# Performance work log

Hardware: AMD Instinct MI355X
Metric: run time of the kernel (lower is better)

## Reference

```python
import jax, jax.numpy as jnp
import numpy as np

B, A, G = 16, 262144, 128


def _make_boxes(key, shape):
    # boxes in (x1, y1, x2, y2) with strictly positive width/height
    k1, k2 = jax.random.split(key)
    cxy = jax.random.uniform(k1, shape[:-1] + (2,), minval=0.0, maxval=1024.0)
    wh = jax.random.uniform(k2, shape[:-1] + (2,), minval=8.0, maxval=256.0)
    return jnp.concatenate([cxy - 0.5 * wh, cxy + 0.5 * wh], axis=-1).astype(jnp.float32)


def setup_inputs() -> dict:
    key = jax.random.key(0)
    k1, k2, k3, k4 = jax.random.split(key, 4)
    bbox_regression = jax.random.normal(k1, (B, A, 4), dtype=jnp.float32)
    anchors = _make_boxes(k2, (A, 4))
    gt_boxes = _make_boxes(k3, (B, G, 4))
    # values in [-2, G): negatives are background/ignored, >=0 index into gt_boxes
    matched_idxs = jax.random.randint(k4, (B, A), -2, G, dtype=jnp.int32)
    return {
        "bbox_regression": bbox_regression,
        "anchors": anchors,
        "gt_boxes": gt_boxes,
        "matched_idxs": matched_idxs,
    }


def _encode(gt, anchors):
    # torchvision BoxCoder.encode_single with weights (1, 1, 1, 1)
    ex_w = anchors[..., 2] - anchors[..., 0]
    ex_h = anchors[..., 3] - anchors[..., 1]
    ex_cx = anchors[..., 0] + 0.5 * ex_w
    ex_cy = anchors[..., 1] + 0.5 * ex_h
    gt_w = gt[..., 2] - gt[..., 0]
    gt_h = gt[..., 3] - gt[..., 1]
    gt_cx = gt[..., 0] + 0.5 * gt_w
    gt_cy = gt[..., 1] + 0.5 * gt_h
    dx = (gt_cx - ex_cx) / ex_w
    dy = (gt_cy - ex_cy) / ex_h
    dw = jnp.log(gt_w / ex_w)
    dh = jnp.log(gt_h / ex_h)
    return jnp.stack([dx, dy, dw, dh], axis=-1)


def reference(bbox_regression, anchors, gt_boxes, matched_idxs):
    fg = matched_idxs >= 0                                  # [B, A] foreground mask
    idx = jnp.maximum(matched_idxs, 0)                      # clamp for safe gather
    matched_gt = jnp.take_along_axis(gt_boxes, idx[..., None], axis=1)  # [B, A, 4]
    target_regression = _encode(matched_gt, anchors[None, :, :])        # [B, A, 4]
    l1 = jnp.sum(jnp.abs(bbox_regression - target_regression), axis=-1)  # [B, A]
    l1 = jnp.where(fg, l1, 0.0)
    num_fg = jnp.sum(fg, axis=1)                            # [B]
    per_image = jnp.sum(l1, axis=1) / jnp.maximum(1, num_fg).astype(l1.dtype)
    return jnp.sum(per_image) / max(1, B)
```

## Files before the change

kernel.cpp:

```cpp
#include <hip/hip_runtime.h>
#include <math.h>

#define BB 16
#define AA 262144
#define GG 128
#define TPB 256
#define NBLK (AA / TPB)
#define RT  1024


__global__ __launch_bounds__(TPB, 3) void loss_main_kernel(
    const float4* __restrict__ reg,
    const float4* __restrict__ anc,
    const float4* __restrict__ gt,
    const int*   __restrict__ mi,
    float2* __restrict__ ws)
{
    __shared__ float4 gts[BB * GG];
    __shared__ float  S[BB][TPB];
    __shared__ float  redC[BB * 4];

    const int t  = threadIdx.x;
    const int bx = blockIdx.x;
    const int a  = bx * TPB + t;

    float4 gload[(BB * GG) / TPB];
#pragma unroll
    for (int i = 0; i < (BB * GG) / TPB; ++i)
        gload[i] = gt[i * TPB + t];

    int mjv[BB];
#pragma unroll
    for (int b = 0; b < BB; ++b) mjv[b] = mi[b * AA + a];

    float4 r[BB];
#pragma unroll
    for (int b = 0; b < BB; ++b) r[b] = reg[b * AA + a];

    const float4 an = anc[a];

#pragma unroll
    for (int i = 0; i < (BB * GG) / TPB; ++i) {
        const float4 g = gload[i];
        const float w = g.z - g.x;
        const float h = g.w - g.y;
        gts[i * TPB + t] = make_float4(g.x + 0.5f * w, g.y + 0.5f * h,
                                       __logf(w), __logf(h));
    }

    const float ex_w  = an.z - an.x;
    const float ex_h  = an.w - an.y;
    const float ex_cx = an.x + 0.5f * ex_w;
    const float ex_cy = an.y + 0.5f * ex_h;
    const float inv_w = 1.0f / ex_w;
    const float inv_h = 1.0f / ex_h;
    const float lw    = __logf(ex_w);
    const float lh    = __logf(ex_h);

    __syncthreads();

    const int wv   = t >> 6;
    const int lane = t & 63;

#pragma unroll
    for (int b = 0; b < BB; ++b) {
        const int mj = mjv[b];
        const float4 g = gts[b * GG + (mj < 0 ? 0 : mj)];

        const float dx = (g.x - ex_cx) * inv_w;
        const float dy = (g.y - ex_cy) * inv_h;
        const float dw = g.z - lw;
        const float dh = g.w - lh;

        const float l1 = fabsf(r[b].x - dx) + fabsf(r[b].y - dy) +
                         fabsf(r[b].z - dw) + fabsf(r[b].w - dh);

        S[b][t] = (mj >= 0) ? l1 : 0.0f;

        const unsigned long long bal = __ballot(mj >= 0);
        if (lane == 0) redC[b * 4 + wv] = (float)__popcll(bal);
    }
    __syncthreads();

    {
        const int b = t >> 4;
        const int c = t & 15;
        float p = 0.0f;
#pragma unroll
        for (int j = 0; j < 16; ++j) p += S[b][c + 16 * j];
#pragma unroll
        for (int o = 8; o > 0; o >>= 1) p += __shfl_down(p, o);
        if (c == 0) {
            const float cnt = redC[b * 4] + redC[b * 4 + 1] +
                              redC[b * 4 + 2] + redC[b * 4 + 3];
            ws[b * NBLK + bx] = make_float2(p, cnt);
        }
    }
}

__global__ __launch_bounds__(RT) void reduce_final_kernel(
    const float2* __restrict__ ws,
    float* __restrict__ out)
{
    __shared__ float per_img[BB];
    const int t    = threadIdx.x;
    const int wv   = t >> 6;
    const int lane = t & 63;

    const float4* w4 = (const float4*)ws;
    float s = 0.0f, c = 0.0f;
#pragma unroll
    for (int k = 0; k < 8; ++k) {
        const float4 v = w4[wv * 512 + k * 64 + lane];
        s += v.x + v.z;
        c += v.y + v.w;
    }
#pragma unroll
    for (int o = 32; o > 0; o >>= 1) {
        s += __shfl_down(s, o);
        c += __shfl_down(c, o);
    }
    if (lane == 0) per_img[wv] = s / fmaxf(1.0f, c);
    __syncthreads();

    if (t == 0) {
        float acc = 0.0f;
#pragma unroll
        for (int b = 0; b < BB; ++b) acc += per_img[b];
        out[0] = acc / (float)BB;
    }
}

extern "C" void kernel_launch(void* const* d_in, const int* in_sizes, int n_in,
                              void* d_out, int out_size, void* d_ws, size_t ws_size,
                              hipStream_t stream) {
    const float4* reg = (const float4*)d_in[0];
    const float4* anc = (const float4*)d_in[1];
    const float4* gt  = (const float4*)d_in[2];
    const int*    mi  = (const int*)d_in[3];

    float2* ws = (float2*)d_ws;

    loss_main_kernel<<<NBLK, TPB, 0, stream>>>(reg, anc, gt, mi, ws);
    reduce_final_kernel<<<1, RT, 0, stream>>>(ws, (float*)d_out);
}
```

Measured before the change: 111.1 us.

## Fuse final reduction into main kernel via cooperative grid sync, two anchors per thread

Replaces the two-kernel launch with a single cooperative kernel in which each thread handles two anchors, halving the block count to 512, and block 0 performs the final reduction after a grid-wide sync. This removes the second kernel launch and amortizes the per-block ground-truth smem preload over more anchors. The cost is doubled register pressure (occupancy hint lowered to 2), the grid-sync overhead, and the requirement that all 512 blocks be co-resident. If the cooperative launch fails, the original two-kernel path runs instead.

Result: slower. 216.0 us (+94.4%).

```diff
diff --git a/kernel.cpp b/kernel.cpp
--- a/kernel.cpp
+++ b/kernel.cpp
@@ -1,13 +1,156 @@
 #include <hip/hip_runtime.h>
+#include <hip/hip_cooperative_groups.h>
 #include <math.h>
+
+namespace cg = cooperative_groups;
 
 #define BB 16
 #define AA 262144
 #define GG 128
 #define TPB 256
-#define NBLK (AA / TPB)
-#define RT  1024
-
+
+#define APBF 512
+#define NBF  (AA / APBF)
+
+#define NBK  (AA / TPB)
+#define RT   1024
+
+__global__ __launch_bounds__(TPB, 2) void loss_fused(
+    const float4* __restrict__ reg,
+    const float4* __restrict__ anc,
+    const float4* __restrict__ gt,
+    const int*   __restrict__ mi,
+    float2* __restrict__ ws,
+    float* __restrict__ out)
+{
+    __shared__ float4 gts[BB * GG];
+    __shared__ float  S[BB][TPB];
+    __shared__ float  redC[BB * 4];
+    __shared__ float  per_img[BB];
+
+    const int t  = threadIdx.x;
+    const int bx = blockIdx.x;
+    const int a0 = bx * APBF + t;
+    const int a1 = a0 + TPB;
+
+    float4 gload[(BB * GG) / TPB];
+#pragma unroll
+    for (int i = 0; i < (BB * GG) / TPB; ++i)
+        gload[i] = gt[i * TPB + t];
+
+    int mj0[BB], mj1[BB];
+#pragma unroll
+    for (int b = 0; b < BB; ++b) mj0[b] = mi[b * AA + a0];
+#pragma unroll
+    for (int b = 0; b < BB; ++b) mj1[b] = mi[b * AA + a1];
+
+    float4 r0[BB], r1[BB];
+#pragma unroll
+    for (int b = 0; b < BB; ++b) r0[b] = reg[b * AA + a0];
+#pragma unroll
+    for (int b = 0; b < BB; ++b) r1[b] = reg[b * AA + a1];
+
+    const float4 an0 = anc[a0];
+    const float4 an1 = anc[a1];
+
+#pragma unroll
+    for (int i = 0; i < (BB * GG) / TPB; ++i) {
+        const float4 g = gload[i];
+        const float w = g.z - g.x;
+        const float h = g.w - g.y;
+        gts[i * TPB + t] = make_float4(g.x + 0.5f * w, g.y + 0.5f * h,
+                                       __logf(w), __logf(h));
+    }
+
+    const float ew0 = an0.z - an0.x, eh0 = an0.w - an0.y;
+    const float cx0 = an0.x + 0.5f * ew0, cy0 = an0.y + 0.5f * eh0;
+    const float iw0 = 1.0f / ew0, ih0 = 1.0f / eh0;
+    const float lw0 = __logf(ew0), lh0 = __logf(eh0);
+
+    const float ew1 = an1.z - an1.x, eh1 = an1.w - an1.y;
+    const float cx1 = an1.x + 0.5f * ew1, cy1 = an1.y + 0.5f * eh1;
+    const float iw1 = 1.0f / ew1, ih1 = 1.0f / eh1;
+    const float lw1 = __logf(ew1), lh1 = __logf(eh1);
+
+    __syncthreads();
+
+    const int wv   = t >> 6;
+    const int lane = t & 63;
+
+#pragma unroll
+    for (int b = 0; b < BB; ++b) {
+        const int m0 = mj0[b];
+        const int m1 = mj1[b];
+        const float4 g0 = gts[b * GG + (m0 < 0 ? 0 : m0)];
+        const float4 g1 = gts[b * GG + (m1 < 0 ? 0 : m1)];
+
+        const float l1a = fabsf(r0[b].x - (g0.x - cx0) * iw0) +
+                          fabsf(r0[b].y - (g0.y - cy0) * ih0) +
+                          fabsf(r0[b].z - (g0.z - lw0)) +
+                          fabsf(r0[b].w - (g0.w - lh0));
+        const float l1b = fabsf(r1[b].x - (g1.x - cx1) * iw1) +
+                          fabsf(r1[b].y - (g1.y - cy1) * ih1) +
+                          fabsf(r1[b].z - (g1.z - lw1)) +
+                          fabsf(r1[b].w - (g1.w - lh1));
+
+        S[b][t] = ((m0 >= 0) ? l1a : 0.0f) + ((m1 >= 0) ? l1b : 0.0f);
+
+        const unsigned long long bal0 = __ballot(m0 >= 0);
+        const unsigned long long bal1 = __ballot(m1 >= 0);
+        if (lane == 0)
+            redC[b * 4 + wv] = (float)(__popcll(bal0) + __popcll(bal1));
+    }
+    __syncthreads();
+
+    {
+        const int b = t >> 4;
+        const int c = t & 15;
+        float p = 0.0f;
+#pragma unroll
+        for (int j = 0; j < 16; ++j) p += S[b][c + 16 * j];
+#pragma unroll
+        for (int o = 8; o > 0; o >>= 1) p += __shfl_down(p, o);
+        if (c == 0) {
+            const float cnt = redC[b * 4] + redC[b * 4 + 1] +
+                              redC[b * 4 + 2] + redC[b * 4 + 3];
+            ws[b * NBF + bx] = make_float2(p, cnt);
+        }
+    }
+
+    __threadfence();
+    cg::this_grid().sync();
+    if (bx != 0) return;
+    __threadfence();
+
+    {
+        const float4* w4 = (const float4*)ws;
+#pragma unroll
+        for (int k = 0; k < 4; ++k) {
+            const int b = wv * 4 + k;
+            float s = 0.0f, c = 0.0f;
+#pragma unroll
+            for (int j = 0; j < 4; ++j) {
+                const float4 v = w4[b * 256 + j * 64 + lane];
+                s += v.x + v.z;
+                c += v.y + v.w;
+            }
+#pragma unroll
+            for (int o = 32; o > 0; o >>= 1) {
+                s += __shfl_down(s, o);
+                c += __shfl_down(c, o);
+            }
+            if (lane == 0) per_img[b] = s / fmaxf(1.0f, c);
+        }
+    }
+    __syncthreads();
+
+    if (t == 0) {
+        float acc = 0.0f;
+#pragma unroll
+        for (int b = 0; b < BB; ++b) acc += per_img[b];
+        out[0] = acc / (float)BB;
+    }
+}
 
 __global__ __launch_bounds__(TPB, 3) void loss_main_kernel(
     const float4* __restrict__ reg,
@@ -93,7 +236,7 @@
         if (c == 0) {
             const float cnt = redC[b * 4] + redC[b * 4 + 1] +
                               redC[b * 4 + 2] + redC[b * 4 + 3];
-            ws[b * NBLK + bx] = make_float2(p, cnt);
+            ws[b * NBK + bx] = make_float2(p, cnt);
         }
     }
 }
@@ -138,9 +281,18 @@
     const float4* anc = (const float4*)d_in[1];
     const float4* gt  = (const float4*)d_in[2];
     const int*    mi  = (const int*)d_in[3];
-
-    float2* ws = (float2*)d_ws;
-
-    loss_main_kernel<<<NBLK, TPB, 0, stream>>>(reg, anc, gt, mi, ws);
-    reduce_final_kernel<<<1, RT, 0, stream>>>(ws, (float*)d_out);
-}
+    float2*       ws  = (float2*)d_ws;
+    float*        o   = (float*)d_out;
+
+    void* args[] = {(void*)&reg, (void*)&anc, (void*)&gt,
+                    (void*)&mi, (void*)&ws, (void*)&o};
+    const hipError_t e = hipLaunchCooperativeKernel(
+        reinterpret_cast<void*>(loss_fused), dim3(NBF), dim3(TPB),
+        args, 0, stream);
+
+    if (e != hipSuccess) {
+        (void)hipGetLastError();
+        loss_main_kernel<<<NBK, TPB, 0, stream>>>(reg, anc, gt, mi, ws);
+        reduce_final_kernel<<<1, RT, 0, stream>>>(ws, o);
+    }
+}
```

## Fuse final reduction into main kernel via block-0 spin-wait on per-block tags

Applied to the files above, without the earlier changes.

Drops the separate reduction kernel launch. Each block publishes its partials and then release-stores a tag derived from the previous output value. Block 0 spins until all 1024 tags match, then reduces the partials and writes the result. This removes a kernel launch and its gap, but block 0 busy-waits while holding a CU slot. Correctness depends on the tag changing between calls (it is derived from the old out value) and on all blocks being co-resident or scheduled eventually; the 1<<20 iteration cap limits how long it can hang.

Result: slower. 188.3 us (+69.5%).

```diff
diff --git a/kernel.cpp b/kernel.cpp
--- a/kernel.cpp
+++ b/kernel.cpp
@@ -6,23 +6,30 @@
 #define GG 128
 #define TPB 256
 #define NBLK (AA / TPB)
-#define RT  1024
+
+typedef unsigned long long ull;
 
 
-__global__ __launch_bounds__(TPB, 3) void loss_main_kernel(
+__global__ __launch_bounds__(TPB, 3) void loss_fused_spin(
     const float4* __restrict__ reg,
     const float4* __restrict__ anc,
     const float4* __restrict__ gt,
     const int*   __restrict__ mi,
-    float2* __restrict__ ws)
+    float2* __restrict__ ws_part,
+    ull*    __restrict__ ws_tag,
+    float* __restrict__ out)
 {
     __shared__ float4 gts[BB * GG];
     __shared__ float  S[BB][TPB];
     __shared__ float  redC[BB * 4];
+    __shared__ float  per_img[BB];
 
     const int t  = threadIdx.x;
     const int bx = blockIdx.x;
     const int a  = bx * TPB + t;
+
+    const unsigned eb = __float_as_uint(out[0]);
+    const ull tagv = ((ull)(eb ^ 0x9E3779B9u) << 32) | (ull)(eb ^ 0x7F4A7C15u);
 
     float4 gload[(BB * GG) / TPB];
 #pragma unroll
@@ -93,34 +100,56 @@
         if (c == 0) {
             const float cnt = redC[b * 4] + redC[b * 4 + 1] +
                               redC[b * 4 + 2] + redC[b * 4 + 3];
-            ws[b * NBLK + bx] = make_float2(p, cnt);
+            ws_part[b * NBLK + bx] = make_float2(p, cnt);
         }
     }
-}
 
-__global__ __launch_bounds__(RT) void reduce_final_kernel(
-    const float2* __restrict__ ws,
-    float* __restrict__ out)
-{
-    __shared__ float per_img[BB];
-    const int t    = threadIdx.x;
-    const int wv   = t >> 6;
-    const int lane = t & 63;
+    __syncthreads();
+    if (t == 0) {
+        __threadfence();
+        __hip_atomic_store(&ws_tag[bx], tagv, __ATOMIC_RELEASE,
+                           __HIP_MEMORY_SCOPE_AGENT);
+    }
+    if (bx != 0) return;
 
-    const float4* w4 = (const float4*)ws;
-    float s = 0.0f, c = 0.0f;
+    {
+        bool all;
+        int sw = 0;
+        do {
+            int ok = 1;
 #pragma unroll
-    for (int k = 0; k < 8; ++k) {
-        const float4 v = w4[wv * 512 + k * 64 + lane];
-        s += v.x + v.z;
-        c += v.y + v.w;
+            for (int k = 0; k < 4; ++k) {
+                const ull v = __hip_atomic_load(&ws_tag[t * 4 + k],
+                                                __ATOMIC_RELAXED,
+                                                __HIP_MEMORY_SCOPE_AGENT);
+                ok &= (v == tagv) ? 1 : 0;
+            }
+            all = (__syncthreads_count(ok) == TPB);
+            if (!all) __builtin_amdgcn_s_sleep(2);
+        } while (!all && ++sw < (1 << 20));
     }
+    __threadfence();
+
+    {
+        const float4* w4 = (const float4*)ws_part;
 #pragma unroll
-    for (int o = 32; o > 0; o >>= 1) {
-        s += __shfl_down(s, o);
-        c += __shfl_down(c, o);
+        for (int k = 0; k < 4; ++k) {
+            const int b = wv * 4 + k;
+            float s = 0.0f, c = 0.0f;
+#pragma unroll
+            for (int j = 0; j < 8; ++j) {
+                const float4 v = w4[b * 512 + j * 64 + lane];
+                s += v.x + v.z;
+                c += v.y + v.w;
+            }
+#pragma unroll
+            for (int o = 32; o > 0; o >>= 1) {
+                s += __shfl_down(s, o);
+                c += __shfl_down(c, o);
+            }
+            if (lane == 0) per_img[b] = s / fmaxf(1.0f, c);
+        }
     }
-    if (lane == 0) per_img[wv] = s / fmaxf(1.0f, c);
     __syncthreads();
 
     if (t == 0) {
@@ -139,8 +168,9 @@
     const float4* gt  = (const float4*)d_in[2];
     const int*    mi  = (const int*)d_in[3];
 
-    float2* ws = (float2*)d_ws;
+    float2* ws_part = (float2*)d_ws;
+    ull*    ws_tag  = (ull*)((char*)d_ws + (size_t)BB * NBLK * sizeof(float2));
 
-    loss_main_kernel<<<NBLK, TPB, 0, stream>>>(reg, anc, gt, mi, ws);
-    reduce_final_kernel<<<1, RT, 0, stream>>>(ws, (float*)d_out);
+    loss_fused_spin<<<NBLK, TPB, 0, stream>>>(reg, anc, gt, mi,
+                                              ws_part, ws_tag, (float*)d_out);
 }
```
